# Optimization experiments

Hardware: AMD Instinct MI355X
Metric: run time of the kernel (lower is better)

Reference implementation:

```python
import jax, jax.numpy as jnp
import numpy as np

EPS = 1e-05
KEEP_RATIO = 0.7


def setup_inputs() -> dict:
    key = jax.random.key(0)
    ks = jax.random.split(key, 10)
    B, C, L, H = 8, 512, 8192, 128
    return {
        "x": jax.random.normal(ks[0], (B, C, L), dtype=jnp.float32),
        "c": jax.random.normal(ks[1], (B, C, L), dtype=jnp.float32),
        "gw1": jax.random.normal(ks[2], (H, C), dtype=jnp.float32) * 0.05,
        "gb1": jax.random.normal(ks[3], (H,), dtype=jnp.float32) * 0.05,
        "gw2": jax.random.normal(ks[4], (C, H), dtype=jnp.float32) * 0.05,
        "gb2": jax.random.normal(ks[5], (C,), dtype=jnp.float32) * 0.05,
        "mw1": jax.random.normal(ks[6], (H, C), dtype=jnp.float32) * 0.05,
        "mb1": jax.random.normal(ks[7], (H,), dtype=jnp.float32) * 0.05,
        "mw2": jax.random.normal(ks[8], (2 * C, H), dtype=jnp.float32) * 0.05,
        "mb2": jax.random.normal(ks[9], (2 * C,), dtype=jnp.float32) * 0.05,
    }


def reference(x, c, gw1, gb1, gw2, gb2, mw1, mb1, mw2, mb2):
    B, C, L = x.shape
    # per-channel stats over L
    mu_c = jnp.mean(x, axis=2, keepdims=True)                 # [B,C,1]
    var_c = jnp.var(x, axis=2, keepdims=True)                 # ddof=0
    sigma_c = jnp.sqrt(var_c + EPS)
    # per-sample stats over (C,L)
    mu_l = jnp.mean(x, axis=(1, 2), keepdims=True)            # [B,1,1]
    var_l = jnp.var(x, axis=(1, 2), keepdims=True)
    sigma_l = jnp.sqrt(var_l + EPS)
    # gate network on c (1x1 convs == channel matmuls), then mean over L
    h = jax.nn.relu(jnp.einsum('hc,bcl->bhl', gw1, c) + gb1[None, :, None])
    g = jax.nn.sigmoid(jnp.einsum('ch,bhl->bcl', gw2, h) + gb2[None, :, None])
    g_mix = jnp.mean(g, axis=2, keepdims=True)                # [B,C,1]
    mu = g_mix * mu_c + (1.0 - g_mix) * mu_l
    sigma = g_mix * sigma_c + (1.0 - g_mix) * sigma_l
    x_hat = (x - mu) / sigma
    # MLP on pooled condition -> gamma, beta
    cond_pool = jnp.mean(c, axis=2)                           # [B,C]
    hm = jax.nn.relu(jnp.einsum('hc,bc->bh', mw1, cond_pool) + mb1)
    gamma_beta = jnp.einsum('oh,bh->bo', mw2, hm) + mb2       # [B,2C]
    gamma = gamma_beta[:, :C][:, :, None]                     # [B,C,1]
    beta = gamma_beta[:, C:][:, :, None]
    y = (1.0 + gamma) * x_hat + beta
    # top-k channel mask by mean |y| over L
    imp = jnp.mean(jnp.abs(y), axis=2)                        # [B,C]
    k = max(1, int(C * KEEP_RATIO))
    _, idx = jax.lax.top_k(imp, k)                            # [B,k]
    mask = jnp.zeros((B, C), dtype=y.dtype).at[jnp.arange(B)[:, None], idx].set(1.0)
    return y * mask[:, :, None]
```

## Files before the change

kernel.cpp:

```cpp
#include <hip/hip_runtime.h>
#include <hip/hip_bf16.h>
#include <math.h>

#define NB 8
#define NC 512
#define NL 8192
#define NH 128
#define FEPS 1e-5f
#define NKEEP 358

typedef __attribute__((ext_vector_type(8))) short short8;
typedef __attribute__((ext_vector_type(4))) float f32x4;

__device__ __forceinline__ unsigned short f2bf(float x) {
  unsigned u = __float_as_uint(x);
  return (unsigned short)((u + 0x7fffu + ((u >> 16) & 1u)) >> 16);
}
__device__ __forceinline__ unsigned pack2(float a, float b) {
  return (unsigned)f2bf(a) | ((unsigned)f2bf(b) << 16);
}

__global__ __launch_bounds__(256) void k0_prep(
    const float* __restrict__ gw1, const float* __restrict__ gw2,
    unsigned short* __restrict__ gw1b, unsigned short* __restrict__ gw2b,
    float* __restrict__ csum, float* __restrict__ gsum) {
  int i = blockIdx.x * 256 + threadIdx.x;
  gw1b[i] = f2bf(gw1[i]);
  gw2b[i] = f2bf(gw2[i]);
  if (i < NB * NC) { csum[i] = 0.f; gsum[i] = 0.f; }
}

__global__ __launch_bounds__(256, 2) void k12_gate_x(
    const float* __restrict__ cin, const float* __restrict__ x,
    const unsigned short* __restrict__ gw1b, const unsigned short* __restrict__ gw2b,
    const float* __restrict__ gb1, const float* __restrict__ gb2,
    float* __restrict__ gsum_g, float* __restrict__ csum_g,
    float* __restrict__ xsum, float* __restrict__ xsumsq) {
  if (blockIdx.x >= 512) {
    const int bc = blockIdx.x - 512;
    const int t = threadIdx.x;
    const float4* xp = reinterpret_cast<const float4*>(x + (size_t)bc * NL);
    float s1 = 0.f, s2 = 0.f;
#pragma unroll
    for (int i = 0; i < 8; ++i) {
      float4 v = xp[i * 256 + t];
      s1 += v.x + v.y + v.z + v.w;
      s2 += v.x * v.x + v.y * v.y + v.z * v.z + v.w * v.w;
    }
    for (int off = 32; off; off >>= 1) { s1 += __shfl_down(s1, off); s2 += __shfl_down(s2, off); }
    __shared__ float r1x[4], r2x[4];
    if ((t & 63) == 0) { r1x[t >> 6] = s1; r2x[t >> 6] = s2; }
    __syncthreads();
    if (t == 0) {
      xsum[bc]   = r1x[0] + r1x[1] + r1x[2] + r1x[3];
      xsumsq[bc] = r2x[0] + r2x[1] + r2x[2] + r2x[3];
    }
    return;
  }

  __shared__ __align__(16) unsigned AsU[2 * 128 * 36];
  __shared__ __align__(16) unsigned short Hts[4][32][136];
  __shared__ float gsum_s[NC], csum_s[NC], gb2_s[NC];
  __shared__ float gb1_s[NH];

  const int t = threadIdx.x;
  const int lane = t & 63;
  const int w = t >> 6;
  const int r = lane & 15;
  const int kg = lane >> 4;
  const int b = blockIdx.x >> 6;
  const int l0 = (blockIdx.x & 63) * 128;

  const int p = t >> 3;
  const int q = t & 7;

  f32x4 acc0[8], acc1[8];
#pragma unroll
  for (int i = 0; i < 8; ++i) { acc0[i] = (f32x4){0.f,0.f,0.f,0.f}; acc1[i] = (f32x4){0.f,0.f,0.f,0.f}; }

  const float* cbase = cin + (size_t)b * NC * NL + l0;
  const unsigned short* gw1r = gw1b + (size_t)r * NC + kg * 8;

  f32x4 vaA[4], vbA[4], vaB[4], vbB[4];

#define LOADA(dA, dB, kch) { \
    _Pragma("unroll") \
    for (int pass = 0; pass < 4; ++pass) { \
      const float* cp0 = cbase + (size_t)((kch) * 64 + 2 * p) * NL + 32 * pass + 4 * q; \
      dA[pass] = __builtin_nontemporal_load(reinterpret_cast<const f32x4*>(cp0)); \
      dB[pass] = __builtin_nontemporal_load(reinterpret_cast<const f32x4*>(cp0 + NL)); \
    } }

#define WRITEA(sA, sB, kch, bufi) { \
    unsigned* dst = AsU + (bufi) * (128 * 36); \
    float sa = 0.f, sb = 0.f; \
    _Pragma("unroll") \
    for (int pass = 0; pass < 4; ++pass) { \
      const int ll = 32 * pass + 4 * q; \
      sa += sA[pass].x + sA[pass].y + sA[pass].z + sA[pass].w; \
      sb += sB[pass].x + sB[pass].y + sB[pass].z + sB[pass].w; \
      dst[(ll + 0) * 36 + p] = pack2(sA[pass].x, sB[pass].x); \
      dst[(ll + 1) * 36 + p] = pack2(sA[pass].y, sB[pass].y); \
      dst[(ll + 2) * 36 + p] = pack2(sA[pass].z, sB[pass].z); \
      dst[(ll + 3) * 36 + p] = pack2(sA[pass].w, sB[pass].w); \
    } \
    sa += __shfl_xor(sa, 1); sa += __shfl_xor(sa, 2); sa += __shfl_xor(sa, 4); \
    sb += __shfl_xor(sb, 1); sb += __shfl_xor(sb, 2); sb += __shfl_xor(sb, 4); \
    if ((lane & 7) == 0) { \
      atomicAdd(&csum_s[(kch) * 64 + 2 * p],     sa); \
      atomicAdd(&csum_s[(kch) * 64 + 2 * p + 1], sb); \
    } }

  LOADA(vaA, vbA, 0)
  LOADA(vaB, vbB, 1)
  for (int i = t; i < NC; i += 256) { gsum_s[i] = 0.f; csum_s[i] = 0.f; gb2_s[i] = gb2[i]; }
  if (t < NH) gb1_s[t] = gb1[t];
  __syncthreads();
  WRITEA(vaA, vbA, 0, 0)
  asm volatile("s_waitcnt lgkmcnt(0)" ::: "memory");
  __builtin_amdgcn_s_barrier();
  __builtin_amdgcn_sched_barrier(0);

  for (int k = 0; k < 8; ++k) {
    const unsigned* Abuf = AsU + (k & 1) * (128 * 36);
    short8 bfr[16];
#pragma unroll
    for (int ht = 0; ht < 8; ++ht) {
      bfr[2 * ht]     = *reinterpret_cast<const short8*>(gw1r + (size_t)(ht * 16) * NC + k * 64);
      bfr[2 * ht + 1] = *reinterpret_cast<const short8*>(gw1r + (size_t)(ht * 16) * NC + k * 64 + 32);
    }
    short8 a0[2], a1[2];
#pragma unroll
    for (int kk = 0; kk < 2; ++kk) {
      a0[kk] = *reinterpret_cast<const short8*>(&Abuf[(32 * w + r)      * 36 + 16 * kk + 4 * kg]);
      a1[kk] = *reinterpret_cast<const short8*>(&Abuf[(32 * w + 16 + r) * 36 + 16 * kk + 4 * kg]);
    }
    __builtin_amdgcn_sched_barrier(0);
    if (k < 7) {
      if ((k & 1) == 0) { WRITEA(vaB, vbB, k + 1, 1) } else { WRITEA(vaA, vbA, k + 1, 0) }
    }
    __builtin_amdgcn_sched_barrier(0);
    if (k < 6) {
      if ((k & 1) == 0) { LOADA(vaA, vbA, k + 2) } else { LOADA(vaB, vbB, k + 2) }
    }
    __builtin_amdgcn_sched_barrier(0);
#pragma unroll
    for (int kk = 0; kk < 2; ++kk) {
#pragma unroll
      for (int ht = 0; ht < 8; ++ht) {
        acc0[ht] = __builtin_amdgcn_mfma_f32_16x16x32_bf16(a0[kk], bfr[2 * ht + kk], acc0[ht], 0, 0, 0);
        acc1[ht] = __builtin_amdgcn_mfma_f32_16x16x32_bf16(a1[kk], bfr[2 * ht + kk], acc1[ht], 0, 0, 0);
      }
    }
    __builtin_amdgcn_sched_barrier(0);
    asm volatile("s_waitcnt lgkmcnt(0)" ::: "memory");
    __builtin_amdgcn_s_barrier();
    __builtin_amdgcn_sched_barrier(0);
  }

#pragma unroll
  for (int ht = 0; ht < 8; ++ht) {
    const float bias = gb1_s[16 * ht + r];
#pragma unroll
    for (int reg = 0; reg < 4; ++reg) {
      Hts[w][4 * kg + reg][16 * ht + r]      = f2bf(fmaxf(acc0[ht][reg] + bias, 0.f));
      Hts[w][16 + 4 * kg + reg][16 * ht + r] = f2bf(fmaxf(acc1[ht][reg] + bias, 0.f));
    }
  }
  short8 af0[4], af1[4];
#pragma unroll
  for (int kk = 0; kk < 4; ++kk) {
    af0[kk] = *reinterpret_cast<const short8*>(&Hts[w][r][32 * kk + 8 * kg]);
    af1[kk] = *reinterpret_cast<const short8*>(&Hts[w][16 + r][32 * kk + 8 * kg]);
  }

  unsigned short* Bs2 = reinterpret_cast<unsigned short*>(AsU);
  const int crow = lane >> 4;
  const int bs2  = lane & 15;
  short8 bv[4];

#define LOADB2(ccn) { \
    _Pragma("unroll") \
    for (int j = 0; j < 4; ++j) { \
      const int cl = 16 * w + 4 * j + crow; \
      bv[j] = *reinterpret_cast<const short8*>(gw2b + (size_t)((ccn) * 64 + cl) * NH + bs2 * 8); \
    } }
#define WRITEB2(ccn) { \
    unsigned short* dstb = Bs2 + ((ccn) & 1) * 8192; \
    _Pragma("unroll") \
    for (int j = 0; j < 4; ++j) { \
      const int cl = 16 * w + 4 * j + crow; \
      *reinterpret_cast<short8*>(&dstb[cl * 128 + ((bs2 ^ (cl & 7)) * 8)]) = bv[j]; \
    } }

  LOADB2(0)
  WRITEB2(0)
  __syncthreads();
  for (int cc = 0; cc < 8; ++cc) {
    if (cc < 7) LOADB2(cc + 1)
    const unsigned short* Bbuf = Bs2 + (cc & 1) * 8192;
#pragma unroll
    for (int ctt = 0; ctt < 4; ++ctt) {
      f32x4 z0 = (f32x4){0.f,0.f,0.f,0.f}, z1 = (f32x4){0.f,0.f,0.f,0.f};
#pragma unroll
      for (int kk = 0; kk < 4; ++kk) {
        const short8 bf = *reinterpret_cast<const short8*>(
            &Bbuf[(16 * ctt + r) * 128 + (((4 * kk + kg) ^ (r & 7)) * 8)]);
        z0 = __builtin_amdgcn_mfma_f32_16x16x32_bf16(af0[kk], bf, z0, 0, 0, 0);
        z1 = __builtin_amdgcn_mfma_f32_16x16x32_bf16(af1[kk], bf, z1, 0, 0, 0);
      }
      const float bias = gb2_s[cc * 64 + 16 * ctt + r];
      float s = 0.f;
#pragma unroll
      for (int reg = 0; reg < 4; ++reg) {
        s += 1.f / (1.f + __expf(-(z0[reg] + bias)));
        s += 1.f / (1.f + __expf(-(z1[reg] + bias)));
      }
      s += __shfl_xor(s, 16);
      s += __shfl_xor(s, 32);
      if (lane < 16) atomicAdd(&gsum_s[cc * 64 + 16 * ctt + lane], s);
    }
    if (cc < 7) WRITEB2(cc + 1)
    __syncthreads();
  }
  for (int i = t; i < NC; i += 256) {
    atomicAdd(&gsum_g[b * NC + i], gsum_s[i]);
    atomicAdd(&csum_g[b * NC + i], csum_s[i]);
  }
}

__global__ __launch_bounds__(256) void k3_final(
    const float* __restrict__ xsum, const float* __restrict__ xsumsq,
    const float* __restrict__ csum, const float* __restrict__ gsum,
    const float* __restrict__ mw1, const float* __restrict__ mb1,
    const float* __restrict__ mw2, const float* __restrict__ mb2,
    float* __restrict__ a_arr, float* __restrict__ d_arr) {
  __shared__ __align__(16) float cp[NC];
  __shared__ __align__(16) float hm[NH];
  __shared__ float gbv[2 * NC];
  __shared__ double red[8];
  __shared__ float mu_l_s, sig_l_s;
  const int b = blockIdx.x, t = threadIdx.x;

  double s1 = 0.0, s2 = 0.0;
  for (int c = t; c < NC; c += 256) { s1 += (double)xsum[b * NC + c]; s2 += (double)xsumsq[b * NC + c]; }
  for (int off = 32; off; off >>= 1) { s1 += __shfl_down(s1, off); s2 += __shfl_down(s2, off); }
  if ((t & 63) == 0) { red[(t >> 6) * 2] = s1; red[(t >> 6) * 2 + 1] = s2; }
  for (int c = t; c < NC; c += 256) cp[c] = csum[b * NC + c] * (1.f / NL);
  __syncthreads();
  if (t == 0) {
    double S1 = red[0] + red[2] + red[4] + red[6];
    double S2 = red[1] + red[3] + red[5] + red[7];
    double n = (double)NC * NL;
    double mu = S1 / n;
    double var = S2 / n - mu * mu;
    mu_l_s = (float)mu;
    sig_l_s = (float)sqrt(var + (double)FEPS);
  }
  __syncthreads();
  if (t < NH) {
    const float4* row = reinterpret_cast<const float4*>(mw1 + (size_t)t * NC);
    const float4* cpv = reinterpret_cast<const float4*>(cp);
    float acc = mb1[t];
    for (int i = 0; i < NC / 4; ++i) {
      float4 wv = row[i], xv = cpv[i];
      acc += wv.x * xv.x + wv.y * xv.y + wv.z * xv.z + wv.w * xv.w;
    }
    hm[t] = fmaxf(acc, 0.f);
  }
  __syncthreads();
  for (int o = t; o < 2 * NC; o += 256) {
    const float4* row = reinterpret_cast<const float4*>(mw2 + (size_t)o * NH);
    const float4* hv = reinterpret_cast<const float4*>(hm);
    float acc = mb2[o];
    for (int i = 0; i < NH / 4; ++i) {
      float4 wv = row[i], xv = hv[i];
      acc += wv.x * xv.x + wv.y * xv.y + wv.z * xv.z + wv.w * xv.w;
    }
    gbv[o] = acc;
  }
  __syncthreads();
  const float mu_l = mu_l_s, sig_l = sig_l_s;
  for (int c = t; c < NC; c += 256) {
    float gm = gsum[b * NC + c] * (1.f / NL);
    double mu_c = (double)xsum[b * NC + c] / NL;
    double var_c = (double)xsumsq[b * NC + c] / NL - mu_c * mu_c;
    float sig_c = (float)sqrt(var_c + (double)FEPS);
    float mu = gm * (float)mu_c + (1.f - gm) * mu_l;
    float sg = gm * sig_c + (1.f - gm) * sig_l;
    float gamma = gbv[c], beta = gbv[NC + c];
    float A = (1.f + gamma) / sg;
    a_arr[b * NC + c] = A;
    d_arr[b * NC + c] = beta - A * mu;
  }
}

__global__ __launch_bounds__(256) void k4_y(
    const float* __restrict__ x, const float* __restrict__ a_arr,
    const float* __restrict__ d_arr, float* __restrict__ out, float* __restrict__ imp) {
  const int bc = blockIdx.x, t = threadIdx.x;
  const float A = a_arr[bc], D = d_arr[bc];
  const f32x4* xp = reinterpret_cast<const f32x4*>(x + (size_t)bc * NL);
  f32x4* op = reinterpret_cast<f32x4*>(out + (size_t)bc * NL);
  float s = 0.f;
#pragma unroll
  for (int i = 0; i < 8; ++i) {
    f32x4 v = __builtin_nontemporal_load(xp + i * 256 + t);
    f32x4 y;
    y.x = fmaf(A, v.x, D); y.y = fmaf(A, v.y, D);
    y.z = fmaf(A, v.z, D); y.w = fmaf(A, v.w, D);
    s += fabsf(y.x) + fabsf(y.y) + fabsf(y.z) + fabsf(y.w);
    __builtin_nontemporal_store(y, op + i * 256 + t);
  }
  for (int off = 32; off; off >>= 1) s += __shfl_down(s, off);
  __shared__ float rs[4];
  if ((t & 63) == 0) rs[t >> 6] = s;
  __syncthreads();
  if (t == 0) imp[bc] = rs[0] + rs[1] + rs[2] + rs[3];
}

__global__ __launch_bounds__(256) void k5_apply(
    const float* __restrict__ imp, float* __restrict__ out) {
  const int bc = blockIdx.x;
  const int b = bc >> 9;
  const int c = bc & (NC - 1);
  const int t = threadIdx.x;
  const float* row = imp + b * NC;
  const float mine = row[c];
  int cnt = 0;
#pragma unroll
  for (int jj = 0; jj < 2; ++jj) {
    const int j = jj * 256 + t;
    const float o = row[j];
    cnt += (o > mine) || (o == mine && j < c);
  }
  for (int off = 32; off; off >>= 1) cnt += __shfl_down(cnt, off);
  __shared__ int rs[4];
  if ((t & 63) == 0) rs[t >> 6] = cnt;
  __syncthreads();
  const int rank = rs[0] + rs[1] + rs[2] + rs[3];
  if (rank < NKEEP) return;
  f32x4* op = reinterpret_cast<f32x4*>(out + (size_t)bc * NL);
  const f32x4 z = (f32x4){0.f, 0.f, 0.f, 0.f};
#pragma unroll
  for (int i = 0; i < 8; ++i) __builtin_nontemporal_store(z, op + i * 256 + t);
}

extern "C" void kernel_launch(void* const* d_in, const int* in_sizes, int n_in,
                              void* d_out, int out_size, void* d_ws, size_t ws_size,
                              hipStream_t stream) {
  const float* x   = (const float*)d_in[0];
  const float* c   = (const float*)d_in[1];
  const float* gw1 = (const float*)d_in[2];
  const float* gb1 = (const float*)d_in[3];
  const float* gw2 = (const float*)d_in[4];
  const float* gb2 = (const float*)d_in[5];
  const float* mw1 = (const float*)d_in[6];
  const float* mb1 = (const float*)d_in[7];
  const float* mw2 = (const float*)d_in[8];
  const float* mb2 = (const float*)d_in[9];
  float* out = (float*)d_out;
  char* ws = (char*)d_ws;

  unsigned short* gw1b = (unsigned short*)(ws);
  unsigned short* gw2b = (unsigned short*)(ws + 131072);
  float* xsum   = (float*)(ws + 262144);
  float* xsumsq = (float*)(ws + 278528);
  float* csum   = (float*)(ws + 294912);
  float* gsum   = (float*)(ws + 311296);
  float* a_arr  = (float*)(ws + 327680);
  float* d_arr  = (float*)(ws + 344064);
  float* imp    = (float*)(ws + 360448);

  k0_prep<<<256, 256, 0, stream>>>(gw1, gw2, gw1b, gw2b, csum, gsum);
  k12_gate_x<<<512 + NB * NC, 256, 0, stream>>>(c, x, gw1b, gw2b, gb1, gb2,
                                                gsum, csum, xsum, xsumsq);
  k3_final<<<NB, 256, 0, stream>>>(xsum, xsumsq, csum, gsum, mw1, mb1, mw2, mb2, a_arr, d_arr);
  k4_y<<<NB * NC, 256, 0, stream>>>(x, a_arr, d_arr, out, imp);
  k5_apply<<<NB * NC, 256, 0, stream>>>(imp, out);
}
```

Measured before the change: 164.9 us.

## Warp-specialize gate kernel: add x-stats waves alongside MFMA gate waves

The separate x-statistics blocks are removed. Each 512-thread block now runs four gate waves doing the MFMA pipeline and four extra waves that stream 8 rows of x and accumulate sum and sum of squares, interleaved at the existing barriers. The aim is to overlap the memory-bound x reduction with the compute-heavy gate work and to drop the tail launch of 4096 small blocks. The risks are higher register and LDS pressure under the launch bound of 512 threads with 4 blocks per CU, and x waves that stall on barriers tied to the gate pipeline.

New measurement: 334.6 us. +102.9%, slower.

```diff
diff --git a/kernel.cpp b/kernel.cpp
--- a/kernel.cpp
+++ b/kernel.cpp
@@ -30,34 +30,12 @@
   if (i < NB * NC) { csum[i] = 0.f; gsum[i] = 0.f; }
 }
 
-__global__ __launch_bounds__(256, 2) void k12_gate_x(
+__global__ __launch_bounds__(512, 4) void k12_gate_x(
     const float* __restrict__ cin, const float* __restrict__ x,
     const unsigned short* __restrict__ gw1b, const unsigned short* __restrict__ gw2b,
     const float* __restrict__ gb1, const float* __restrict__ gb2,
     float* __restrict__ gsum_g, float* __restrict__ csum_g,
     float* __restrict__ xsum, float* __restrict__ xsumsq) {
-  if (blockIdx.x >= 512) {
-    const int bc = blockIdx.x - 512;
-    const int t = threadIdx.x;
-    const float4* xp = reinterpret_cast<const float4*>(x + (size_t)bc * NL);
-    float s1 = 0.f, s2 = 0.f;
-#pragma unroll
-    for (int i = 0; i < 8; ++i) {
-      float4 v = xp[i * 256 + t];
-      s1 += v.x + v.y + v.z + v.w;
-      s2 += v.x * v.x + v.y * v.y + v.z * v.z + v.w * v.w;
-    }
-    for (int off = 32; off; off >>= 1) { s1 += __shfl_down(s1, off); s2 += __shfl_down(s2, off); }
-    __shared__ float r1x[4], r2x[4];
-    if ((t & 63) == 0) { r1x[t >> 6] = s1; r2x[t >> 6] = s2; }
-    __syncthreads();
-    if (t == 0) {
-      xsum[bc]   = r1x[0] + r1x[1] + r1x[2] + r1x[3];
-      xsumsq[bc] = r2x[0] + r2x[1] + r2x[2] + r2x[3];
-    }
-    return;
-  }
-
   __shared__ __align__(16) unsigned AsU[2 * 128 * 36];
   __shared__ __align__(16) unsigned short Hts[4][32][136];
   __shared__ float gsum_s[NC], csum_s[NC], gb2_s[NC];
@@ -66,6 +44,7 @@
   const int t = threadIdx.x;
   const int lane = t & 63;
   const int w = t >> 6;
+  const bool isGate = (w < 4);
   const int r = lane & 15;
   const int kg = lane >> 4;
   const int b = blockIdx.x >> 6;
@@ -82,6 +61,18 @@
   const unsigned short* gw1r = gw1b + (size_t)r * NC + kg * 8;
 
   f32x4 vaA[4], vbA[4], vaB[4], vbB[4];
+
+  unsigned short* Bs2 = reinterpret_cast<unsigned short*>(AsU);
+  const int crow = lane >> 4;
+  const int bs2  = lane & 15;
+  short8 bv[4];
+  short8 af0[4], af1[4];
+
+  const int xw = w - 4;
+  const f32x4* xv0 = reinterpret_cast<const f32x4*>(x + ((size_t)blockIdx.x * 8 + 2 * xw) * NL);
+  const f32x4* xv1 = xv0 + (NL / 4);
+  f32x4 xb0, xb1, xb2, xb3;
+  float s1a = 0.f, s2a = 0.f, s1b = 0.f, s2b = 0.f;
 
 #define LOADA(dA, dB, kch) { \
     _Pragma("unroll") \
@@ -111,73 +102,100 @@
       atomicAdd(&csum_s[(kch) * 64 + 2 * p + 1], sb); \
     } }
 
-  LOADA(vaA, vbA, 0)
-  LOADA(vaB, vbB, 1)
-  for (int i = t; i < NC; i += 256) { gsum_s[i] = 0.f; csum_s[i] = 0.f; gb2_s[i] = gb2[i]; }
-  if (t < NH) gb1_s[t] = gb1[t];
-  __syncthreads();
-  WRITEA(vaA, vbA, 0, 0)
-  asm volatile("s_waitcnt lgkmcnt(0)" ::: "memory");
+#define XISSUE(i) { \
+    xb0 = xv0[(i) * 128 + lane]; \
+    xb1 = xv0[(i) * 128 + 64 + lane]; \
+    xb2 = xv1[(i) * 128 + lane]; \
+    xb3 = xv1[(i) * 128 + 64 + lane]; }
+
+#define XACCUM() { \
+    s1a += xb0.x + xb0.y + xb0.z + xb0.w + xb1.x + xb1.y + xb1.z + xb1.w; \
+    s2a += xb0.x * xb0.x + xb0.y * xb0.y + xb0.z * xb0.z + xb0.w * xb0.w \
+         + xb1.x * xb1.x + xb1.y * xb1.y + xb1.z * xb1.z + xb1.w * xb1.w; \
+    s1b += xb2.x + xb2.y + xb2.z + xb2.w + xb3.x + xb3.y + xb3.z + xb3.w; \
+    s2b += xb2.x * xb2.x + xb2.y * xb2.y + xb2.z * xb2.z + xb2.w * xb2.w \
+         + xb3.x * xb3.x + xb3.y * xb3.y + xb3.z * xb3.z + xb3.w * xb3.w; }
+
+  if (isGate) {
+    LOADA(vaA, vbA, 0)
+    LOADA(vaB, vbB, 1)
+    for (int i = t; i < NC; i += 256) { gsum_s[i] = 0.f; csum_s[i] = 0.f; gb2_s[i] = gb2[i]; }
+    if (t < NH) gb1_s[t] = gb1[t];
+  } else {
+    XISSUE(0)
+  }
+  __syncthreads();
+  if (isGate) {
+    WRITEA(vaA, vbA, 0, 0)
+    asm volatile("s_waitcnt lgkmcnt(0)" ::: "memory");
+  } else {
+    XACCUM()
+    XISSUE(1)
+  }
   __builtin_amdgcn_s_barrier();
   __builtin_amdgcn_sched_barrier(0);
 
   for (int k = 0; k < 8; ++k) {
-    const unsigned* Abuf = AsU + (k & 1) * (128 * 36);
-    short8 bfr[16];
-#pragma unroll
-    for (int ht = 0; ht < 8; ++ht) {
-      bfr[2 * ht]     = *reinterpret_cast<const short8*>(gw1r + (size_t)(ht * 16) * NC + k * 64);
-      bfr[2 * ht + 1] = *reinterpret_cast<const short8*>(gw1r + (size_t)(ht * 16) * NC + k * 64 + 32);
-    }
-    short8 a0[2], a1[2];
-#pragma unroll
-    for (int kk = 0; kk < 2; ++kk) {
-      a0[kk] = *reinterpret_cast<const short8*>(&Abuf[(32 * w + r)      * 36 + 16 * kk + 4 * kg]);
-      a1[kk] = *reinterpret_cast<const short8*>(&Abuf[(32 * w + 16 + r) * 36 + 16 * kk + 4 * kg]);
-    }
-    __builtin_amdgcn_sched_barrier(0);
-    if (k < 7) {
-      if ((k & 1) == 0) { WRITEA(vaB, vbB, k + 1, 1) } else { WRITEA(vaA, vbA, k + 1, 0) }
-    }
-    __builtin_amdgcn_sched_barrier(0);
-    if (k < 6) {
-      if ((k & 1) == 0) { LOADA(vaA, vbA, k + 2) } else { LOADA(vaB, vbB, k + 2) }
-    }
-    __builtin_amdgcn_sched_barrier(0);
-#pragma unroll
-    for (int kk = 0; kk < 2; ++kk) {
+    if (isGate) {
+      const unsigned* Abuf = AsU + (k & 1) * (128 * 36);
+      short8 bfr[16];
 #pragma unroll
       for (int ht = 0; ht < 8; ++ht) {
-        acc0[ht] = __builtin_amdgcn_mfma_f32_16x16x32_bf16(a0[kk], bfr[2 * ht + kk], acc0[ht], 0, 0, 0);
-        acc1[ht] = __builtin_amdgcn_mfma_f32_16x16x32_bf16(a1[kk], bfr[2 * ht + kk], acc1[ht], 0, 0, 0);
-      }
-    }
-    __builtin_amdgcn_sched_barrier(0);
-    asm volatile("s_waitcnt lgkmcnt(0)" ::: "memory");
+        bfr[2 * ht]     = *reinterpret_cast<const short8*>(gw1r + (size_t)(ht * 16) * NC + k * 64);
+        bfr[2 * ht + 1] = *reinterpret_cast<const short8*>(gw1r + (size_t)(ht * 16) * NC + k * 64 + 32);
+      }
+      short8 a0[2], a1[2];
+#pragma unroll
+      for (int kk = 0; kk < 2; ++kk) {
+        a0[kk] = *reinterpret_cast<const short8*>(&Abuf[(32 * w + r)      * 36 + 16 * kk + 4 * kg]);
+        a1[kk] = *reinterpret_cast<const short8*>(&Abuf[(32 * w + 16 + r) * 36 + 16 * kk + 4 * kg]);
+      }
+      __builtin_amdgcn_sched_barrier(0);
+      if (k < 7) {
+        if ((k & 1) == 0) { WRITEA(vaB, vbB, k + 1, 1) } else { WRITEA(vaA, vbA, k + 1, 0) }
+      }
+      __builtin_amdgcn_sched_barrier(0);
+      if (k < 6) {
+        if ((k & 1) == 0) { LOADA(vaA, vbA, k + 2) } else { LOADA(vaB, vbB, k + 2) }
+      }
+      __builtin_amdgcn_sched_barrier(0);
+#pragma unroll
+      for (int kk = 0; kk < 2; ++kk) {
+#pragma unroll
+        for (int ht = 0; ht < 8; ++ht) {
+          acc0[ht] = __builtin_amdgcn_mfma_f32_16x16x32_bf16(a0[kk], bfr[2 * ht + kk], acc0[ht], 0, 0, 0);
+          acc1[ht] = __builtin_amdgcn_mfma_f32_16x16x32_bf16(a1[kk], bfr[2 * ht + kk], acc1[ht], 0, 0, 0);
+        }
+      }
+      __builtin_amdgcn_sched_barrier(0);
+      asm volatile("s_waitcnt lgkmcnt(0)" ::: "memory");
+    } else {
+      XACCUM()
+      XISSUE(k + 2)
+    }
     __builtin_amdgcn_s_barrier();
     __builtin_amdgcn_sched_barrier(0);
   }
 
-#pragma unroll
-  for (int ht = 0; ht < 8; ++ht) {
-    const float bias = gb1_s[16 * ht + r];
-#pragma unroll
-    for (int reg = 0; reg < 4; ++reg) {
-      Hts[w][4 * kg + reg][16 * ht + r]      = f2bf(fmaxf(acc0[ht][reg] + bias, 0.f));
-      Hts[w][16 + 4 * kg + reg][16 * ht + r] = f2bf(fmaxf(acc1[ht][reg] + bias, 0.f));
-    }
-  }
-  short8 af0[4], af1[4];
-#pragma unroll
-  for (int kk = 0; kk < 4; ++kk) {
-    af0[kk] = *reinterpret_cast<const short8*>(&Hts[w][r][32 * kk + 8 * kg]);
-    af1[kk] = *reinterpret_cast<const short8*>(&Hts[w][16 + r][32 * kk + 8 * kg]);
-  }
-
-  unsigned short* Bs2 = reinterpret_cast<unsigned short*>(AsU);
-  const int crow = lane >> 4;
-  const int bs2  = lane & 15;
-  short8 bv[4];
+  if (isGate) {
+#pragma unroll
+    for (int ht = 0; ht < 8; ++ht) {
+      const float bias = gb1_s[16 * ht + r];
+#pragma unroll
+      for (int reg = 0; reg < 4; ++reg) {
+        Hts[w][4 * kg + reg][16 * ht + r]      = f2bf(fmaxf(acc0[ht][reg] + bias, 0.f));
+        Hts[w][16 + 4 * kg + reg][16 * ht + r] = f2bf(fmaxf(acc1[ht][reg] + bias, 0.f));
+      }
+    }
+#pragma unroll
+    for (int kk = 0; kk < 4; ++kk) {
+      af0[kk] = *reinterpret_cast<const short8*>(&Hts[w][r][32 * kk + 8 * kg]);
+      af1[kk] = *reinterpret_cast<const short8*>(&Hts[w][16 + r][32 * kk + 8 * kg]);
+    }
+  } else {
+    XACCUM()
+    XISSUE(10)
+  }
 
 #define LOADB2(ccn) { \
     _Pragma("unroll") \
@@ -193,39 +211,58 @@
       *reinterpret_cast<short8*>(&dstb[cl * 128 + ((bs2 ^ (cl & 7)) * 8)]) = bv[j]; \
     } }
 
-  LOADB2(0)
-  WRITEB2(0)
+  if (isGate) {
+    LOADB2(0)
+    WRITEB2(0)
+  }
   __syncthreads();
   for (int cc = 0; cc < 8; ++cc) {
-    if (cc < 7) LOADB2(cc + 1)
-    const unsigned short* Bbuf = Bs2 + (cc & 1) * 8192;
-#pragma unroll
-    for (int ctt = 0; ctt < 4; ++ctt) {
-      f32x4 z0 = (f32x4){0.f,0.f,0.f,0.f}, z1 = (f32x4){0.f,0.f,0.f,0.f};
-#pragma unroll
-      for (int kk = 0; kk < 4; ++kk) {
-        const short8 bf = *reinterpret_cast<const short8*>(
-            &Bbuf[(16 * ctt + r) * 128 + (((4 * kk + kg) ^ (r & 7)) * 8)]);
-        z0 = __builtin_amdgcn_mfma_f32_16x16x32_bf16(af0[kk], bf, z0, 0, 0, 0);
-        z1 = __builtin_amdgcn_mfma_f32_16x16x32_bf16(af1[kk], bf, z1, 0, 0, 0);
-      }
-      const float bias = gb2_s[cc * 64 + 16 * ctt + r];
-      float s = 0.f;
-#pragma unroll
-      for (int reg = 0; reg < 4; ++reg) {
-        s += 1.f / (1.f + __expf(-(z0[reg] + bias)));
-        s += 1.f / (1.f + __expf(-(z1[reg] + bias)));
-      }
-      s += __shfl_xor(s, 16);
-      s += __shfl_xor(s, 32);
-      if (lane < 16) atomicAdd(&gsum_s[cc * 64 + 16 * ctt + lane], s);
-    }
-    if (cc < 7) WRITEB2(cc + 1)
+    if (isGate) {
+      if (cc < 7) LOADB2(cc + 1)
+      const unsigned short* Bbuf = Bs2 + (cc & 1) * 8192;
+#pragma unroll
+      for (int ctt = 0; ctt < 4; ++ctt) {
+        f32x4 z0 = (f32x4){0.f,0.f,0.f,0.f}, z1 = (f32x4){0.f,0.f,0.f,0.f};
+#pragma unroll
+        for (int kk = 0; kk < 4; ++kk) {
+          const short8 bf = *reinterpret_cast<const short8*>(
+              &Bbuf[(16 * ctt + r) * 128 + (((4 * kk + kg) ^ (r & 7)) * 8)]);
+          z0 = __builtin_amdgcn_mfma_f32_16x16x32_bf16(af0[kk], bf, z0, 0, 0, 0);
+          z1 = __builtin_amdgcn_mfma_f32_16x16x32_bf16(af1[kk], bf, z1, 0, 0, 0);
+        }
+        const float bias = gb2_s[cc * 64 + 16 * ctt + r];
+        float s = 0.f;
+#pragma unroll
+        for (int reg = 0; reg < 4; ++reg) {
+          s += 1.f / (1.f + __expf(-(z0[reg] + bias)));
+          s += 1.f / (1.f + __expf(-(z1[reg] + bias)));
+        }
+        s += __shfl_xor(s, 16);
+        s += __shfl_xor(s, 32);
+        if (lane < 16) atomicAdd(&gsum_s[cc * 64 + 16 * ctt + lane], s);
+      }
+      if (cc < 7) WRITEB2(cc + 1)
+    } else {
+      if (cc < 6) { XACCUM() }
+      if (cc < 5) { XISSUE(11 + cc) }
+    }
     __syncthreads();
   }
-  for (int i = t; i < NC; i += 256) {
-    atomicAdd(&gsum_g[b * NC + i], gsum_s[i]);
-    atomicAdd(&csum_g[b * NC + i], csum_s[i]);
+  if (isGate) {
+    for (int i = t; i < NC; i += 256) {
+      atomicAdd(&gsum_g[b * NC + i], gsum_s[i]);
+      atomicAdd(&csum_g[b * NC + i], csum_s[i]);
+    }
+  } else {
+    for (int off = 32; off; off >>= 1) {
+      s1a += __shfl_down(s1a, off); s2a += __shfl_down(s2a, off);
+      s1b += __shfl_down(s1b, off); s2b += __shfl_down(s2b, off);
+    }
+    if (lane == 0) {
+      const size_t row = (size_t)blockIdx.x * 8 + 2 * xw;
+      xsum[row]       = s1a; xsumsq[row]     = s2a;
+      xsum[row + 1]   = s1b; xsumsq[row + 1] = s2b;
+    }
   }
 }
 
@@ -373,8 +410,8 @@
   float* imp    = (float*)(ws + 360448);
 
   k0_prep<<<256, 256, 0, stream>>>(gw1, gw2, gw1b, gw2b, csum, gsum);
-  k12_gate_x<<<512 + NB * NC, 256, 0, stream>>>(c, x, gw1b, gw2b, gb1, gb2,
-                                                gsum, csum, xsum, xsumsq);
+  k12_gate_x<<<512, 512, 0, stream>>>(c, x, gw1b, gw2b, gb1, gb2,
+                                      gsum, csum, xsum, xsumsq);
   k3_final<<<NB, 256, 0, stream>>>(xsum, xsumsq, csum, gsum, mw1, mb1, mw2, mb2, a_arr, d_arr);
   k4_y<<<NB * NC, 256, 0, stream>>>(x, a_arr, d_arr, out, imp);
   k5_apply<<<NB * NC, 256, 0, stream>>>(imp, out);
```
